# Kernel optimization log

Hardware: AMD Instinct MI355X
Metric: run time of the kernel (lower is better)

The kernel has to match this reference:

```python
import jax, jax.numpy as jnp
import numpy as np

DELTA_V = 0.1
DELTA_D = 0.5
NUM_LABELS = 33  # label 0 = background, instance ids 1..32


def setup_inputs() -> dict:
    key = jax.random.key(0)
    k1, k2 = jax.random.split(key)
    B, N, D = 8, 131072, 32
    embeddings = jax.random.normal(k1, (B, N, D), dtype=jnp.float32)
    labels = jax.random.randint(k2, (B, N), 0, NUM_LABELS, dtype=jnp.int32)
    return {"embeddings": embeddings, "labels": labels}


def reference(embeddings, labels):
    # embeddings: [B, N, D], labels: [B, N] int (0 = ignore)
    B = embeddings.shape[0]
    dt = embeddings.dtype

    oh = jax.nn.one_hot(labels, NUM_LABELS, dtype=dt)              # [B, N, L]
    counts = oh.sum(1)                                              # [B, L]
    sums = jnp.einsum('bnl,bnd->bld', oh, embeddings)               # [B, L, D]
    means = sums / jnp.maximum(counts, 1.0)[..., None]              # [B, L, D]

    # ---- pull loss: hinge on distance of each point to its instance mean ----
    mean_pt = jnp.take_along_axis(means, labels[..., None], axis=1)  # [B, N, D]
    diff = embeddings - mean_pt
    dist = jnp.sqrt(jnp.sum(diff * diff, -1) + 1e-24)               # [B, N]
    hinge = jnp.maximum(dist - DELTA_V, 0.0)
    seg_mean = jnp.einsum('bnl,bn->bl', oh, hinge) / jnp.maximum(counts, 1.0)  # [B, L]

    present = counts[:, 1:] > 0                                     # [B, L-1]
    n_inst = present.sum(-1).astype(dt)                             # [B]
    pull_b = seg_mean[:, 1:].sum(-1) / (n_inst + 1e-6)
    pull = pull_b.sum() / B

    # ---- push loss: hinge margin between normalized instance means ----
    m = means[:, 1:, :]                                             # [B, L-1, D]
    mn = m / jnp.maximum(jnp.linalg.norm(m, axis=-1, keepdims=True), 1e-12)
    sq = jnp.sum((mn[:, :, None, :] - mn[:, None, :, :]) ** 2, -1)  # [B, K, K]
    dmat = jnp.sqrt(sq + 1e-24)
    K = NUM_LABELS - 1
    triu = jnp.triu(jnp.ones((K, K), dt), 1)
    pmask = triu[None] * present[:, :, None].astype(dt) * present[:, None, :].astype(dt)
    hp = jnp.maximum(2.0 * DELTA_D - dmat, 0.0) * pmask
    push_b = jnp.where(n_inst > 1, hp.sum((-2, -1)) / (pmask.sum((-2, -1)) + 1e-6), 0.0)
    push = push_b.sum() / B

    total = pull + push
    return jnp.stack([total, pull, push])
```

## Files before the change

### kernel.cpp

```cpp
#include <hip/hip_runtime.h>
#include <hip/hip_bf16.h>

#define BATCH 8
#define NPTS  131072
#define DIM   32
#define NLAB  33
#define G1X   256
#define P1PTS 512
#define BPB2  128

#define OFF_CNT   0
#define OFF_SUM   264
#define OFF_PULL  (264 + 8448)
#define OFF_PSUM  (OFF_PULL + BATCH * BPB2)
#define OFF_PCNT  (OFF_PSUM + BATCH * G1X * NLAB * DIM)
#define WS_FLOATS (OFF_PCNT + BATCH * G1X * NLAB)

typedef short  bf16x8 __attribute__((ext_vector_type(8)));
typedef float  f32x4  __attribute__((ext_vector_type(4)));

static __device__ __forceinline__ short f2bf(float f) {
  __hip_bfloat16 h = __float2bfloat16(f);
  return *reinterpret_cast<short*>(&h);
}

__global__ __launch_bounds__(256) void pass1_kernel(
    const float* __restrict__ emb, const int* __restrict__ lab,
    float* __restrict__ psum, float* __restrict__ pcnt) {
  const int b    = blockIdx.y;
  const int tid  = threadIdx.x;
  const int w    = tid >> 6;
  const int lane = tid & 63;

  constexpr int STEPS = P1PTS / 128;

  __shared__ float s_stage[4][32 * 33];
  __shared__ int   s_cnt4[4][NLAB];
  float* st = s_stage[w];

  const size_t base = (size_t)b * NPTS + (size_t)blockIdx.x * P1PTS
                    + (size_t)w * (P1PTS / 4);

  const int m0 = lane & 15;
  const int g  = lane >> 4;
  f32x4 acc[3][2];
#pragma unroll
  for (int t = 0; t < 3; ++t)
#pragma unroll
    for (int u = 0; u < 2; ++u) acc[t][u] = (f32x4){0.f, 0.f, 0.f, 0.f};
  int cnt0 = 0, cnt1 = 0, cnt2 = 0;

  float4 ld[4];
  int labv;
  {
    const float4* src = (const float4*)(emb + base * DIM);
#pragma unroll
    for (int r = 0; r < 4; ++r) ld[r] = src[lane + 64 * r];
    labv = lab[base + (lane & 31)];
  }

  for (int step = 0; step < STEPS; ++step) {
#pragma unroll
    for (int r = 0; r < 4; ++r) {
      const int i = lane + 64 * r;
      const int p = i >> 3, d0 = (i & 7) * 4;
      st[(d0 + 0) * 33 + p] = ld[r].x;
      st[(d0 + 1) * 33 + p] = ld[r].y;
      st[(d0 + 2) * 33 + p] = ld[r].z;
      st[(d0 + 3) * 33 + p] = ld[r].w;
    }
    const int labv_c = labv;

    if (step < STEPS - 1) {
      const float4* src = (const float4*)(emb + (base + (step + 1) * 32) * DIM);
#pragma unroll
      for (int r = 0; r < 4; ++r) ld[r] = src[lane + 64 * r];
      labv = lab[base + (step + 1) * 32 + (lane & 31)];
    }

    bf16x8 a0, a1, a2;
#pragma unroll
    for (int j = 0; j < 8; ++j) {
      const int lj = __shfl(labv_c, g * 8 + j);
      const int h0 = (lj == m0), h1 = (lj == m0 + 16), h2 = (lj == m0 + 32);
      a0[j] = h0 ? (short)0x3F80 : (short)0;
      a1[j] = h1 ? (short)0x3F80 : (short)0;
      a2[j] = h2 ? (short)0x3F80 : (short)0;
      cnt0 += h0; cnt1 += h1; cnt2 += h2;
    }

    bf16x8 b0, b1;
#pragma unroll
    for (int j = 0; j < 8; ++j) {
      b0[j] = f2bf(st[m0 * 33 + g * 8 + j]);
      b1[j] = f2bf(st[(m0 + 16) * 33 + g * 8 + j]);
    }

    acc[0][0] = __builtin_amdgcn_mfma_f32_16x16x32_bf16(a0, b0, acc[0][0], 0, 0, 0);
    acc[0][1] = __builtin_amdgcn_mfma_f32_16x16x32_bf16(a0, b1, acc[0][1], 0, 0, 0);
    acc[1][0] = __builtin_amdgcn_mfma_f32_16x16x32_bf16(a1, b0, acc[1][0], 0, 0, 0);
    acc[1][1] = __builtin_amdgcn_mfma_f32_16x16x32_bf16(a1, b1, acc[1][1], 0, 0, 0);
    acc[2][0] = __builtin_amdgcn_mfma_f32_16x16x32_bf16(a2, b0, acc[2][0], 0, 0, 0);
    acc[2][1] = __builtin_amdgcn_mfma_f32_16x16x32_bf16(a2, b1, acc[2][1], 0, 0, 0);
  }

  cnt0 += __shfl_xor(cnt0, 16); cnt0 += __shfl_xor(cnt0, 32);
  cnt1 += __shfl_xor(cnt1, 16); cnt1 += __shfl_xor(cnt1, 32);
  cnt2 += __shfl_xor(cnt2, 16); cnt2 += __shfl_xor(cnt2, 32);
  if (lane < 16)            s_cnt4[w][m0]      = cnt0;
  else if (lane < 32)       s_cnt4[w][m0 + 16] = cnt1;
  if (lane == 32)           s_cnt4[w][32]      = cnt2;

#pragma unroll
  for (int t = 0; t < 2; ++t)
#pragma unroll
    for (int u = 0; u < 2; ++u)
#pragma unroll
      for (int r = 0; r < 4; ++r)
        st[(t * 16 + g * 4 + r) * DIM + m0 + 16 * u] = acc[t][u][r];
  if (lane < 16) {
    st[32 * DIM + m0]      = acc[2][0][0];
    st[32 * DIM + m0 + 16] = acc[2][1][0];
  }
  __syncthreads();

  const size_t pb = (size_t)b * G1X + blockIdx.x;
  for (int i = tid; i < NLAB * DIM; i += 256) {
    const float v = s_stage[0][i] + s_stage[1][i] + s_stage[2][i] + s_stage[3][i];
    psum[pb * (NLAB * DIM) + i] = v;
  }
  if (tid < NLAB) {
    const int c = s_cnt4[0][tid] + s_cnt4[1][tid] + s_cnt4[2][tid] + s_cnt4[3][tid];
    pcnt[pb * NLAB + tid] = (float)c;
  }
}

__global__ __launch_bounds__(256) void reduce_kernel(
    const float* __restrict__ psum, const float* __restrict__ pcnt,
    float* __restrict__ gsum, float* __restrict__ gcnt) {
  constexpr int TOT = BATCH * NLAB * DIM;
  constexpr int KS  = G1X / 8;
  const int slice = blockIdx.y;
  const int o = blockIdx.x * 256 + threadIdx.x;
  if (o < TOT) {
    const int b = o / (NLAB * DIM), i = o - b * (NLAB * DIM);
    const float* src = psum + ((size_t)b * G1X + slice * KS) * (NLAB * DIM) + i;
    float a0 = 0.f, a1 = 0.f, a2 = 0.f, a3 = 0.f;
#pragma unroll
    for (int k = 0; k < KS; k += 4) {
      a0 += src[(size_t)(k + 0) * (NLAB * DIM)];
      a1 += src[(size_t)(k + 1) * (NLAB * DIM)];
      a2 += src[(size_t)(k + 2) * (NLAB * DIM)];
      a3 += src[(size_t)(k + 3) * (NLAB * DIM)];
    }
    atomicAdd(&gsum[o], (a0 + a1) + (a2 + a3));
  } else if (o - TOT < BATCH * NLAB) {
    const int o2 = o - TOT;
    const int b = o2 / NLAB, l = o2 - b * NLAB;
    const float* src = pcnt + ((size_t)b * G1X + slice * KS) * NLAB + l;
    float a = 0.f;
#pragma unroll
    for (int k = 0; k < KS; ++k) a += src[(size_t)k * NLAB];
    atomicAdd(&gcnt[o2], a);
  }
}

#define CN 8
#define P2_ISSUE(LB, EB, C)                                                   \
  {                                                                           \
    _Pragma("unroll")                                                         \
    for (int j = 0; j < CN; ++j) {                                            \
      const size_t it = (size_t)(C) * CN + j;                                 \
      const unsigned long long al =                                           \
          (unsigned long long)(lab + base + p0 + it * PSTRIDE);               \
      asm volatile("global_load_dword %0, %1, off" : "=&v"(LB[j]) : "v"(al)); \
    }                                                                         \
    _Pragma("unroll")                                                         \
    for (int j = 0; j < CN; ++j) {                                            \
      const size_t it = (size_t)(C) * CN + j;                                 \
      const unsigned long long ae =                                           \
          (unsigned long long)(emb + (base + p0 + it * PSTRIDE) * DIM + d0);  \
      asm volatile("global_load_dwordx4 %0, %1, off" : "=&v"(EB[j]) : "v"(ae)); \
    }                                                                         \
  }

#define P2_COMPUTE(LB, EB)                                                    \
  {                                                                           \
    float s[CN];                                                              \
    _Pragma("unroll")                                                         \
    for (int j = 0; j < CN; ++j) {                                            \
      const f32x4 mv = *(const f32x4*)(s_mean + LB[j] * 36 + d0);             \
      const float dx = EB[j][0] - mv[0], dy = EB[j][1] - mv[1];               \
      const float dz = EB[j][2] - mv[2], dw = EB[j][3] - mv[3];               \
      s[j] = dx * dx + dy * dy + dz * dz + dw * dw;                           \
    }                                                                         \
    _Pragma("unroll")                                                         \
    for (int j = 0; j < CN; ++j) {                                            \
      s[j] += __shfl_xor(s[j], 1);                                            \
      s[j] += __shfl_xor(s[j], 2);                                            \
      s[j] += __shfl_xor(s[j], 4);                                            \
    }                                                                         \
    float sv = s[0];                                                          \
    int   lv = LB[0];                                                         \
    _Pragma("unroll")                                                         \
    for (int j = 1; j < CN; ++j) {                                            \
      sv = (lane8 == j) ? s[j] : sv;                                          \
      lv = (lane8 == j) ? LB[j] : lv;                                         \
    }                                                                         \
    const float dist = sqrtf(sv + 1e-24f);                                    \
    wacc += s_w[lv] * fmaxf(dist - 0.1f, 0.f);                                \
  }

__global__ __launch_bounds__(256, 4) void pass2_kernel(
    const float* __restrict__ emb, const int* __restrict__ lab,
    const float* __restrict__ gsum, const float* __restrict__ gcnt,
    float* __restrict__ pull_part) {
  const int b   = blockIdx.y;
  const int tid = threadIdx.x;
  __shared__ __align__(16) float s_mean[NLAB * 36];
  __shared__ float s_w[NLAB];
  __shared__ float s_red[4];

  for (int i = tid; i < NLAB * DIM; i += 256) {
    const int l = i >> 5, d = i & 31;
    const float c = gcnt[b * NLAB + l];
    s_mean[l * 36 + d] = gsum[b * (NLAB * DIM) + i] / fmaxf(c, 1.0f);
  }
  if (tid < 64) {
    const float c = (tid < NLAB) ? gcnt[b * NLAB + tid] : 0.f;
    const int pres = (tid >= 1 && tid < NLAB && c > 0.f) ? 1 : 0;
    const unsigned long long bal = __ballot(pres);
    const float n_inst = (float)__popcll(bal);
    if (tid < NLAB)
      s_w[tid] = pres ? 1.f / (fmaxf(c, 1.f) * (n_inst + 1e-6f)) : 0.f;
  }
  __syncthreads();

  const int sub   = tid >> 3;
  const int lane8 = tid & 7;
  const int d0    = lane8 << 2;
  const size_t base = (size_t)b * NPTS;
  const int p0 = blockIdx.x * 32 + sub;
  constexpr int PSTRIDE = BPB2 * 32;
  constexpr int NIT     = NPTS / PSTRIDE;
  constexpr int NCH     = NIT / CN;

  int   labsA[CN], labsB[CN];
  f32x4 eA[CN], eB[CN];
  float wacc = 0.f;

  P2_ISSUE(labsA, eA, 0);
#pragma unroll
  for (int cc = 0; cc < NCH; cc += 2) {
    if (cc + 1 < NCH) P2_ISSUE(labsB, eB, cc + 1);
    if (cc + 1 < NCH) { asm volatile("s_waitcnt vmcnt(16)" ::: "memory"); }
    else              { asm volatile("s_waitcnt vmcnt(0)"  ::: "memory"); }
    __builtin_amdgcn_sched_barrier(0);
    P2_COMPUTE(labsA, eA);
    if (cc + 1 < NCH) {
      if (cc + 2 < NCH) P2_ISSUE(labsA, eA, cc + 2);
      if (cc + 2 < NCH) { asm volatile("s_waitcnt vmcnt(16)" ::: "memory"); }
      else              { asm volatile("s_waitcnt vmcnt(0)"  ::: "memory"); }
      __builtin_amdgcn_sched_barrier(0);
      P2_COMPUTE(labsB, eB);
    }
  }

#pragma unroll
  for (int mm = 1; mm < 64; mm <<= 1) wacc += __shfl_xor(wacc, mm);
  if ((tid & 63) == 0) s_red[tid >> 6] = wacc;
  __syncthreads();
  if (tid == 0)
    pull_part[b * BPB2 + blockIdx.x] =
        s_red[0] + s_red[1] + s_red[2] + s_red[3];
}

__global__ __launch_bounds__(512) void finish_kernel(
    const float* __restrict__ gsum, const float* __restrict__ gcnt,
    const float* __restrict__ pull_part, float* __restrict__ out) {
  const int tid = threadIdx.x;
  const int b   = tid >> 6;
  const int t   = tid & 63;
  __shared__ __align__(16) float s_mn[BATCH * 32 * DIM];
  __shared__ float s_ps[BATCH];
  __shared__ float s_pl[BATCH];
  float* mn = s_mn + b * 32 * DIM;

  {
    float plsum = pull_part[b * BPB2 + t] + pull_part[b * BPB2 + 64 + t];
#pragma unroll
    for (int m = 1; m < 64; m <<= 1) plsum += __shfl_xor(plsum, m);
    if (t == 0) s_pl[b] = plsum;
  }

  int pres = 0;
  if (t < 32) {
    const int l = t + 1;
    const float cnt = gcnt[b * NLAB + l];
    pres = (cnt > 0.f) ? 1 : 0;
    const float inv = 1.f / fmaxf(cnt, 1.f);
    float v[DIM];
    float n2 = 0.f;
    for (int d = 0; d < DIM; d++) {
      v[d] = gsum[b * (NLAB * DIM) + l * DIM + d] * inv;
      n2  += v[d] * v[d];
    }
    const float scale = 1.f / fmaxf(sqrtf(n2), 1e-12f);
    for (int d = 0; d < DIM; d++) mn[t * DIM + d] = v[d] * scale;
  }
  const unsigned long long bal = __ballot(pres);
  const unsigned int pmask32 = (unsigned int)(bal & 0xFFFFFFFFull);
  const int n_inst = __popc(pmask32);

  __syncthreads();

  float hp_sum = 0.f, pm_sum = 0.f;
  for (int idx = t; idx < 1024; idx += 64) {
    const int i = idx >> 5, j = idx & 31;
    if (j > i && ((pmask32 >> i) & 1u) && ((pmask32 >> j) & 1u)) {
      const float4* a = (const float4*)(mn + i * DIM);
      const float4* c = (const float4*)(mn + j * DIM);
      float sq = 0.f;
      for (int q = 0; q < 8; q++) {
        const float4 av = a[q], cv = c[q];
        const float dx = av.x - cv.x, dy = av.y - cv.y;
        const float dz = av.z - cv.z, dw = av.w - cv.w;
        sq += dx * dx + dy * dy + dz * dz + dw * dw;
      }
      const float dmat = sqrtf(sq + 1e-24f);
      hp_sum += fmaxf(1.0f - dmat, 0.f);
      pm_sum += 1.f;
    }
  }
  for (int m = 1; m < 64; m <<= 1) {
    hp_sum += __shfl_xor(hp_sum, m);
    pm_sum += __shfl_xor(pm_sum, m);
  }
  const float push = (n_inst > 1) ? hp_sum / (pm_sum + 1e-6f) : 0.f;
  if (t == 0) s_ps[b] = push;
  __syncthreads();

  if (tid < 64) {
    float pl = (t < BATCH) ? s_pl[t] : 0.f;
    float ps = (t < BATCH) ? s_ps[t] : 0.f;
#pragma unroll
    for (int m = 1; m < 64; m <<= 1) {
      pl += __shfl_xor(pl, m);
      ps += __shfl_xor(ps, m);
    }
    if (t == 0) {
      const float pull_m = pl / (float)BATCH;
      const float push_m = ps / (float)BATCH;
      out[0] = pull_m + push_m;
      out[1] = pull_m;
      out[2] = push_m;
    }
  }
}

extern "C" void kernel_launch(void* const* d_in, const int* in_sizes, int n_in,
                              void* d_out, int out_size, void* d_ws, size_t ws_size,
                              hipStream_t stream) {
  const float* emb = (const float*)d_in[0];
  const int*   lab = (const int*)d_in[1];
  float* out = (float*)d_out;
  float* ws  = (float*)d_ws;

  float* gcnt  = ws + OFF_CNT;
  float* gsum  = ws + OFF_SUM;
  float* pullp = ws + OFF_PULL;
  float* psum  = ws + OFF_PSUM;
  float* pcnt  = ws + OFF_PCNT;

  hipMemsetAsync(d_ws, 0, (OFF_SUM + BATCH * NLAB * DIM) * sizeof(float), stream);

  dim3 grid1(G1X, BATCH);
  dim3 gridR((BATCH * NLAB * DIM + BATCH * NLAB + 255) / 256, 8);
  dim3 grid2(BPB2, BATCH);
  pass1_kernel<<<grid1, 256, 0, stream>>>(emb, lab, psum, pcnt);
  reduce_kernel<<<gridR, 256, 0, stream>>>(psum, pcnt, gsum, gcnt);
  pass2_kernel<<<grid2, 256, 0, stream>>>(emb, lab, gsum, gcnt, pullp);
  finish_kernel<<<1, 512, 0, stream>>>(gsum, gcnt, pullp, out);
}
```

Before: 237.1 us.

## Load pass-1 embeddings directly into registers with inline-asm double-buffered pipeline

Pass 1 now loads embedding values straight from global memory into the MFMA B-operand layout with per-dword inline-asm loads. This drops the LDS transpose staging. Two register buffers are double-buffered with explicit vmcnt waits so the next tile's loads overlap the current tile's MFMAs. It also halves the grid by doubling points per block (1024), cutting partial-sum output and the later reduction work. The risks are uncoalesced scalar dword loads, higher register pressure, and lower occupancy from fewer blocks.

```diff
diff --git a/kernel.cpp b/kernel.cpp
--- a/kernel.cpp
+++ b/kernel.cpp
@@ -5,8 +5,8 @@
 #define NPTS  131072
 #define DIM   32
 #define NLAB  33
-#define G1X   256
-#define P1PTS 512
+#define G1X   128
+#define P1PTS 1024
 #define BPB2  128
 
 #define OFF_CNT   0
@@ -24,25 +24,73 @@
   return *reinterpret_cast<short*>(&h);
 }
 
+#define P1_ISSUE(LABD, BV, T)                                                 \
+  {                                                                           \
+    const int vt = vbase + (T) * 4096;                                        \
+    const int vl = lloff + (T) * 128;                                         \
+    asm volatile("global_load_dword %0, %1, %2"                               \
+                 : "=&v"(LABD) : "v"(vl), "s"(lbase));                        \
+    asm volatile("global_load_dword %0, %1, %2"            : "=&v"(BV[0])  : "v"(vt), "s"(ebase)); \
+    asm volatile("global_load_dword %0, %1, %2 offset:128" : "=&v"(BV[1])  : "v"(vt), "s"(ebase)); \
+    asm volatile("global_load_dword %0, %1, %2 offset:256" : "=&v"(BV[2])  : "v"(vt), "s"(ebase)); \
+    asm volatile("global_load_dword %0, %1, %2 offset:384" : "=&v"(BV[3])  : "v"(vt), "s"(ebase)); \
+    asm volatile("global_load_dword %0, %1, %2 offset:512" : "=&v"(BV[4])  : "v"(vt), "s"(ebase)); \
+    asm volatile("global_load_dword %0, %1, %2 offset:640" : "=&v"(BV[5])  : "v"(vt), "s"(ebase)); \
+    asm volatile("global_load_dword %0, %1, %2 offset:768" : "=&v"(BV[6])  : "v"(vt), "s"(ebase)); \
+    asm volatile("global_load_dword %0, %1, %2 offset:896" : "=&v"(BV[7])  : "v"(vt), "s"(ebase)); \
+    asm volatile("global_load_dword %0, %1, %2 offset:64"  : "=&v"(BV[8])  : "v"(vt), "s"(ebase)); \
+    asm volatile("global_load_dword %0, %1, %2 offset:192" : "=&v"(BV[9])  : "v"(vt), "s"(ebase)); \
+    asm volatile("global_load_dword %0, %1, %2 offset:320" : "=&v"(BV[10]) : "v"(vt), "s"(ebase)); \
+    asm volatile("global_load_dword %0, %1, %2 offset:448" : "=&v"(BV[11]) : "v"(vt), "s"(ebase)); \
+    asm volatile("global_load_dword %0, %1, %2 offset:576" : "=&v"(BV[12]) : "v"(vt), "s"(ebase)); \
+    asm volatile("global_load_dword %0, %1, %2 offset:704" : "=&v"(BV[13]) : "v"(vt), "s"(ebase)); \
+    asm volatile("global_load_dword %0, %1, %2 offset:832" : "=&v"(BV[14]) : "v"(vt), "s"(ebase)); \
+    asm volatile("global_load_dword %0, %1, %2 offset:960" : "=&v"(BV[15]) : "v"(vt), "s"(ebase)); \
+  }
+
+#define P1_COMPUTE(LABD, BV)                                                  \
+  {                                                                           \
+    const int labv_c = LABD;                                                  \
+    bf16x8 a0, a1, a2, b0, b1;                                                \
+    _Pragma("unroll")                                                         \
+    for (int j = 0; j < 8; ++j) {                                             \
+      const int lj = __shfl(labv_c, g * 8 + j);                               \
+      const int h0 = (lj == m0), h1 = (lj == m0 + 16), h2 = (lj == m0 + 32);  \
+      a0[j] = h0 ? (short)0x3F80 : (short)0;                                  \
+      a1[j] = h1 ? (short)0x3F80 : (short)0;                                  \
+      a2[j] = h2 ? (short)0x3F80 : (short)0;                                  \
+      cnt0 += h0; cnt1 += h1; cnt2 += h2;                                     \
+      b0[j] = f2bf(BV[j]);                                                    \
+      b1[j] = f2bf(BV[8 + j]);                                                \
+    }                                                                         \
+    acc[0][0] = __builtin_amdgcn_mfma_f32_16x16x32_bf16(a0, b0, acc[0][0], 0, 0, 0); \
+    acc[0][1] = __builtin_amdgcn_mfma_f32_16x16x32_bf16(a0, b1, acc[0][1], 0, 0, 0); \
+    acc[1][0] = __builtin_amdgcn_mfma_f32_16x16x32_bf16(a1, b0, acc[1][0], 0, 0, 0); \
+    acc[1][1] = __builtin_amdgcn_mfma_f32_16x16x32_bf16(a1, b1, acc[1][1], 0, 0, 0); \
+    acc[2][0] = __builtin_amdgcn_mfma_f32_16x16x32_bf16(a2, b0, acc[2][0], 0, 0, 0); \
+    acc[2][1] = __builtin_amdgcn_mfma_f32_16x16x32_bf16(a2, b1, acc[2][1], 0, 0, 0); \
+  }
+
 __global__ __launch_bounds__(256) void pass1_kernel(
     const float* __restrict__ emb, const int* __restrict__ lab,
     float* __restrict__ psum, float* __restrict__ pcnt) {
   const int b    = blockIdx.y;
   const int tid  = threadIdx.x;
-  const int w    = tid >> 6;
+  const int w    = __builtin_amdgcn_readfirstlane(tid >> 6);
   const int lane = tid & 63;
-
-  constexpr int STEPS = P1PTS / 128;
-
-  __shared__ float s_stage[4][32 * 33];
+  const int m0   = lane & 15;
+  const int g    = lane >> 4;
+
+  __shared__ float s_stage[4][NLAB * DIM];
   __shared__ int   s_cnt4[4][NLAB];
-  float* st = s_stage[w];
 
   const size_t base = (size_t)b * NPTS + (size_t)blockIdx.x * P1PTS
-                    + (size_t)w * (P1PTS / 4);
-
-  const int m0 = lane & 15;
-  const int g  = lane >> 4;
+                    + (size_t)w * 256;
+  const float* ebase = emb + base * DIM;
+  const int*   lbase = lab + base;
+  const int vbase = g * 1024 + m0 * 4;
+  const int lloff = (lane & 31) * 4;
+
   f32x4 acc[3][2];
 #pragma unroll
   for (int t = 0; t < 3; ++t)
@@ -50,58 +98,24 @@
     for (int u = 0; u < 2; ++u) acc[t][u] = (f32x4){0.f, 0.f, 0.f, 0.f};
   int cnt0 = 0, cnt1 = 0, cnt2 = 0;
 
-  float4 ld[4];
-  int labv;
-  {
-    const float4* src = (const float4*)(emb + base * DIM);
-#pragma unroll
-    for (int r = 0; r < 4; ++r) ld[r] = src[lane + 64 * r];
-    labv = lab[base + (lane & 31)];
-  }
-
-  for (int step = 0; step < STEPS; ++step) {
-#pragma unroll
-    for (int r = 0; r < 4; ++r) {
-      const int i = lane + 64 * r;
-      const int p = i >> 3, d0 = (i & 7) * 4;
-      st[(d0 + 0) * 33 + p] = ld[r].x;
-      st[(d0 + 1) * 33 + p] = ld[r].y;
-      st[(d0 + 2) * 33 + p] = ld[r].z;
-      st[(d0 + 3) * 33 + p] = ld[r].w;
-    }
-    const int labv_c = labv;
-
-    if (step < STEPS - 1) {
-      const float4* src = (const float4*)(emb + (base + (step + 1) * 32) * DIM);
-#pragma unroll
-      for (int r = 0; r < 4; ++r) ld[r] = src[lane + 64 * r];
-      labv = lab[base + (step + 1) * 32 + (lane & 31)];
-    }
-
-    bf16x8 a0, a1, a2;
-#pragma unroll
-    for (int j = 0; j < 8; ++j) {
-      const int lj = __shfl(labv_c, g * 8 + j);
-      const int h0 = (lj == m0), h1 = (lj == m0 + 16), h2 = (lj == m0 + 32);
-      a0[j] = h0 ? (short)0x3F80 : (short)0;
-      a1[j] = h1 ? (short)0x3F80 : (short)0;
-      a2[j] = h2 ? (short)0x3F80 : (short)0;
-      cnt0 += h0; cnt1 += h1; cnt2 += h2;
-    }
-
-    bf16x8 b0, b1;
-#pragma unroll
-    for (int j = 0; j < 8; ++j) {
-      b0[j] = f2bf(st[m0 * 33 + g * 8 + j]);
-      b1[j] = f2bf(st[(m0 + 16) * 33 + g * 8 + j]);
-    }
-
-    acc[0][0] = __builtin_amdgcn_mfma_f32_16x16x32_bf16(a0, b0, acc[0][0], 0, 0, 0);
-    acc[0][1] = __builtin_amdgcn_mfma_f32_16x16x32_bf16(a0, b1, acc[0][1], 0, 0, 0);
-    acc[1][0] = __builtin_amdgcn_mfma_f32_16x16x32_bf16(a1, b0, acc[1][0], 0, 0, 0);
-    acc[1][1] = __builtin_amdgcn_mfma_f32_16x16x32_bf16(a1, b1, acc[1][1], 0, 0, 0);
-    acc[2][0] = __builtin_amdgcn_mfma_f32_16x16x32_bf16(a2, b0, acc[2][0], 0, 0, 0);
-    acc[2][1] = __builtin_amdgcn_mfma_f32_16x16x32_bf16(a2, b1, acc[2][1], 0, 0, 0);
+  int   labA, labB;
+  float bvA[16], bvB[16];
+
+  P1_ISSUE(labA, bvA, 0);
+#pragma unroll
+  for (int t = 0; t < 8; t += 2) {
+    P1_ISSUE(labB, bvB, t + 1);
+    asm volatile("s_waitcnt vmcnt(17)" ::: "memory");
+    __builtin_amdgcn_sched_barrier(0);
+    P1_COMPUTE(labA, bvA);
+    if (t + 2 < 8) {
+      P1_ISSUE(labA, bvA, t + 2);
+      asm volatile("s_waitcnt vmcnt(17)" ::: "memory");
+    } else {
+      asm volatile("s_waitcnt vmcnt(0)" ::: "memory");
+    }
+    __builtin_amdgcn_sched_barrier(0);
+    P1_COMPUTE(labB, bvB);
   }
 
   cnt0 += __shfl_xor(cnt0, 16); cnt0 += __shfl_xor(cnt0, 32);
@@ -111,6 +125,7 @@
   else if (lane < 32)       s_cnt4[w][m0 + 16] = cnt1;
   if (lane == 32)           s_cnt4[w][32]      = cnt2;
 
+  float* st = s_stage[w];
 #pragma unroll
   for (int t = 0; t < 2; ++t)
 #pragma unroll
```

After: 234.7 us. No clear change (-1.0%).

## Replace MFMA one-hot segment sum with LDS atomic histogram and inline-asm loads

Applied to the files above, without the earlier changes.

Pass1 no longer builds bf16 one-hot matrices and multiplies them with MFMA. Each thread now does float atomicAdds of its embedding chunk into a shared per-label histogram, with counts handled the same way. All loads for the block are issued up front through inline-asm global_load_dwordx4 in two batches, and explicit vmcnt waits overlap the second batch with accumulation of the first. This drops the LDS transpose, the bf16 conversion and its precision loss, but LDS atomics can contend when many points share a label.

```diff
diff --git a/kernel.cpp b/kernel.cpp
--- a/kernel.cpp
+++ b/kernel.cpp
@@ -19,120 +19,74 @@
 typedef short  bf16x8 __attribute__((ext_vector_type(8)));
 typedef float  f32x4  __attribute__((ext_vector_type(4)));
 
-static __device__ __forceinline__ short f2bf(float f) {
-  __hip_bfloat16 h = __float2bfloat16(f);
-  return *reinterpret_cast<short*>(&h);
-}
+#define P1_ISSUE(EB, LB, SR)                                                  \
+  {                                                                           \
+    _Pragma("unroll")                                                         \
+    for (int j = 0; j < 8; ++j) {                                             \
+      const int ve = ve0 + ((SR) * 8 + j) * 4096;                             \
+      const int vl = vl0 + ((SR) * 8 + j) * 128;                              \
+      asm volatile("global_load_dwordx4 %0, %1, %2"                           \
+                   : "=&v"(EB[j]) : "v"(ve), "s"(ebase));                     \
+      asm volatile("global_load_dword %0, %1, %2"                             \
+                   : "=&v"(LB[j]) : "v"(vl), "s"(lbase));                     \
+    }                                                                         \
+  }
+
+#define P1_ACCUM(EB, LB)                                                      \
+  {                                                                           \
+    _Pragma("unroll")                                                         \
+    for (int j = 0; j < 8; ++j) {                                             \
+      const int lb = LB[j];                                                   \
+      float* hp = s_hist + lb * 33 + lane8 * 4;                               \
+      atomicAdd(hp + 0, EB[j][0]);                                            \
+      atomicAdd(hp + 1, EB[j][1]);                                            \
+      atomicAdd(hp + 2, EB[j][2]);                                            \
+      atomicAdd(hp + 3, EB[j][3]);                                            \
+      if (lane8 == 0) atomicAdd(&s_cnt[lb], 1);                               \
+    }                                                                         \
+  }
 
 __global__ __launch_bounds__(256) void pass1_kernel(
     const float* __restrict__ emb, const int* __restrict__ lab,
     float* __restrict__ psum, float* __restrict__ pcnt) {
-  const int b    = blockIdx.y;
-  const int tid  = threadIdx.x;
-  const int w    = tid >> 6;
-  const int lane = tid & 63;
-
-  constexpr int STEPS = P1PTS / 128;
-
-  __shared__ float s_stage[4][32 * 33];
-  __shared__ int   s_cnt4[4][NLAB];
-  float* st = s_stage[w];
-
-  const size_t base = (size_t)b * NPTS + (size_t)blockIdx.x * P1PTS
-                    + (size_t)w * (P1PTS / 4);
-
-  const int m0 = lane & 15;
-  const int g  = lane >> 4;
-  f32x4 acc[3][2];
-#pragma unroll
-  for (int t = 0; t < 3; ++t)
-#pragma unroll
-    for (int u = 0; u < 2; ++u) acc[t][u] = (f32x4){0.f, 0.f, 0.f, 0.f};
-  int cnt0 = 0, cnt1 = 0, cnt2 = 0;
-
-  float4 ld[4];
-  int labv;
-  {
-    const float4* src = (const float4*)(emb + base * DIM);
-#pragma unroll
-    for (int r = 0; r < 4; ++r) ld[r] = src[lane + 64 * r];
-    labv = lab[base + (lane & 31)];
-  }
-
-  for (int step = 0; step < STEPS; ++step) {
-#pragma unroll
-    for (int r = 0; r < 4; ++r) {
-      const int i = lane + 64 * r;
-      const int p = i >> 3, d0 = (i & 7) * 4;
-      st[(d0 + 0) * 33 + p] = ld[r].x;
-      st[(d0 + 1) * 33 + p] = ld[r].y;
-      st[(d0 + 2) * 33 + p] = ld[r].z;
-      st[(d0 + 3) * 33 + p] = ld[r].w;
-    }
-    const int labv_c = labv;
-
-    if (step < STEPS - 1) {
-      const float4* src = (const float4*)(emb + (base + (step + 1) * 32) * DIM);
-#pragma unroll
-      for (int r = 0; r < 4; ++r) ld[r] = src[lane + 64 * r];
-      labv = lab[base + (step + 1) * 32 + (lane & 31)];
-    }
-
-    bf16x8 a0, a1, a2;
-#pragma unroll
-    for (int j = 0; j < 8; ++j) {
-      const int lj = __shfl(labv_c, g * 8 + j);
-      const int h0 = (lj == m0), h1 = (lj == m0 + 16), h2 = (lj == m0 + 32);
-      a0[j] = h0 ? (short)0x3F80 : (short)0;
-      a1[j] = h1 ? (short)0x3F80 : (short)0;
-      a2[j] = h2 ? (short)0x3F80 : (short)0;
-      cnt0 += h0; cnt1 += h1; cnt2 += h2;
-    }
-
-    bf16x8 b0, b1;
-#pragma unroll
-    for (int j = 0; j < 8; ++j) {
-      b0[j] = f2bf(st[m0 * 33 + g * 8 + j]);
-      b1[j] = f2bf(st[(m0 + 16) * 33 + g * 8 + j]);
-    }
-
-    acc[0][0] = __builtin_amdgcn_mfma_f32_16x16x32_bf16(a0, b0, acc[0][0], 0, 0, 0);
-    acc[0][1] = __builtin_amdgcn_mfma_f32_16x16x32_bf16(a0, b1, acc[0][1], 0, 0, 0);
-    acc[1][0] = __builtin_amdgcn_mfma_f32_16x16x32_bf16(a1, b0, acc[1][0], 0, 0, 0);
-    acc[1][1] = __builtin_amdgcn_mfma_f32_16x16x32_bf16(a1, b1, acc[1][1], 0, 0, 0);
-    acc[2][0] = __builtin_amdgcn_mfma_f32_16x16x32_bf16(a2, b0, acc[2][0], 0, 0, 0);
-    acc[2][1] = __builtin_amdgcn_mfma_f32_16x16x32_bf16(a2, b1, acc[2][1], 0, 0, 0);
-  }
-
-  cnt0 += __shfl_xor(cnt0, 16); cnt0 += __shfl_xor(cnt0, 32);
-  cnt1 += __shfl_xor(cnt1, 16); cnt1 += __shfl_xor(cnt1, 32);
-  cnt2 += __shfl_xor(cnt2, 16); cnt2 += __shfl_xor(cnt2, 32);
-  if (lane < 16)            s_cnt4[w][m0]      = cnt0;
-  else if (lane < 32)       s_cnt4[w][m0 + 16] = cnt1;
-  if (lane == 32)           s_cnt4[w][32]      = cnt2;
-
-#pragma unroll
-  for (int t = 0; t < 2; ++t)
-#pragma unroll
-    for (int u = 0; u < 2; ++u)
-#pragma unroll
-      for (int r = 0; r < 4; ++r)
-        st[(t * 16 + g * 4 + r) * DIM + m0 + 16 * u] = acc[t][u][r];
-  if (lane < 16) {
-    st[32 * DIM + m0]      = acc[2][0][0];
-    st[32 * DIM + m0 + 16] = acc[2][1][0];
-  }
+  const int b     = blockIdx.y;
+  const int tid   = threadIdx.x;
+  const int sub   = tid >> 3;
+  const int lane8 = tid & 7;
+
+  __shared__ float s_hist[NLAB * 33];
+  __shared__ int   s_cnt[NLAB];
+
+  for (int i = tid; i < NLAB * 33; i += 256) s_hist[i] = 0.f;
+  if (tid < NLAB) s_cnt[tid] = 0;
+  __syncthreads();
+
+  const size_t base = (size_t)b * NPTS + (size_t)blockIdx.x * P1PTS;
+  const float* ebase = emb + base * DIM;
+  const int*   lbase = lab + base;
+  const int ve0 = sub * 128 + lane8 * 16;
+  const int vl0 = sub * 4;
+
+  f32x4 eA[8], eB[8];
+  int   lA[8], lB[8];
+
+  P1_ISSUE(eA, lA, 0);
+  P1_ISSUE(eB, lB, 1);
+  asm volatile("s_waitcnt vmcnt(16)" ::: "memory");
+  __builtin_amdgcn_sched_barrier(0);
+  P1_ACCUM(eA, lA);
+  asm volatile("s_waitcnt vmcnt(0)" ::: "memory");
+  __builtin_amdgcn_sched_barrier(0);
+  P1_ACCUM(eB, lB);
+
   __syncthreads();
 
   const size_t pb = (size_t)b * G1X + blockIdx.x;
   for (int i = tid; i < NLAB * DIM; i += 256) {
-    const float v = s_stage[0][i] + s_stage[1][i] + s_stage[2][i] + s_stage[3][i];
-    psum[pb * (NLAB * DIM) + i] = v;
-  }
-  if (tid < NLAB) {
-    const int c = s_cnt4[0][tid] + s_cnt4[1][tid] + s_cnt4[2][tid] + s_cnt4[3][tid];
-    pcnt[pb * NLAB + tid] = (float)c;
-  }
+    const int l = i >> 5, d = i & 31;
+    psum[pb * (NLAB * DIM) + i] = s_hist[l * 33 + d];
+  }
+  if (tid < NLAB) pcnt[pb * NLAB + tid] = (float)s_cnt[tid];
 }
 
 __global__ __launch_bounds__(256) void reduce_kernel(
```

Measured after the change: 363.1 us. 1.53x slower.
